# Performance work log

Hardware: AMD Instinct MI355X
Metric: run time of the kernel (lower is better)

## Reference

```python
import jax, jax.numpy as jnp
import numpy as np

DIM = 1024
DEPTH = 4
HEADS = 16
MLP_DIM = 4096
EPS = 1e-5


def layer_norm(x, g, b):
    mu = jnp.mean(x, axis=-1, keepdims=True)
    var = jnp.mean(jnp.square(x - mu), axis=-1, keepdims=True)
    return (x - mu) * jax.lax.rsqrt(var + EPS) * g + b


def setup_inputs() -> dict:
    key = jax.random.key(0)
    ks = jax.random.split(key, 8)
    s = DIM ** -0.5
    return {
        "x": jax.random.normal(ks[0], (2, 1024, DIM), dtype=jnp.float32),
        "ln1_g": jnp.ones((DIM,), jnp.float32),
        "ln1_b": jnp.zeros((DIM,), jnp.float32),
        "w_qkv": jax.random.normal(ks[1], (DIM, 3 * DIM), jnp.float32) * s,
        "w_o": jax.random.normal(ks[2], (DIM, DIM), jnp.float32) * s,
        "b_o": jnp.zeros((DIM,), jnp.float32),
        "ln2_g": jnp.ones((DIM,), jnp.float32),
        "ln2_b": jnp.zeros((DIM,), jnp.float32),
        "w1": jax.random.normal(ks[3], (DIM, MLP_DIM), jnp.float32) * s,
        "b1": jnp.zeros((MLP_DIM,), jnp.float32),
        "w2": jax.random.normal(ks[4], (MLP_DIM, DIM), jnp.float32) * (MLP_DIM ** -0.5),
        "b2": jnp.zeros((DIM,), jnp.float32),
    }


def reference(x, ln1_g, ln1_b, w_qkv, w_o, b_o, ln2_g, ln2_b, w1, b1, w2, b2):
    b, n, _ = x.shape
    h, d = HEADS, DIM // HEADS
    scale = DIM ** -0.5  # NB: full dim, as in source
    for _ in range(DEPTH):  # same (shared) weights each layer, per ModuleList([m]*depth)
        # --- attention with pre-norm + residual ---
        xn = layer_norm(x, ln1_g, ln1_b)
        qkv = xn @ w_qkv  # [b, n, 3*dim]
        qkv = qkv.reshape(b, n, 3, h, d)
        q = qkv[:, :, 0].transpose(0, 2, 1, 3)  # [b, h, n, d]
        k = qkv[:, :, 1].transpose(0, 2, 1, 3)
        v = qkv[:, :, 2].transpose(0, 2, 1, 3)
        scores = jnp.einsum('bhid,bhjd->bhij', q, k) * scale
        attn = jax.nn.softmax(scores, axis=-1)
        out = jnp.einsum('bhij,bhjd->bhid', attn, v)
        out = out.transpose(0, 2, 1, 3).reshape(b, n, DIM)
        x = out @ w_o + b_o + x
        # --- MLP with pre-norm + residual ---
        xn = layer_norm(x, ln2_g, ln2_b)
        hdn = jax.nn.gelu(xn @ w1 + b1, approximate=False)
        x = hdn @ w2 + b2 + x
    return x
```

## Files before the change

### kernel.cpp

```cpp
#include <hip/hip_runtime.h>
#include <math.h>

#define NTOK 2048
#define DIM_ 1024
#define NSEQ 1024
#define HEADS_ 16
#define HD 64
#define MLP_ 4096
#define EPS_ 1e-5f

#define FLAG_BIAS  1
#define FLAG_GELU  2
#define FLAG_QKV   8
#define FLAG_PART  16

typedef __attribute__((ext_vector_type(8))) short bf16x8;
typedef __attribute__((ext_vector_type(4))) float f32x4;
typedef __attribute__((ext_vector_type(16))) float f32x16;

__device__ __forceinline__ unsigned short f2bf(float f) {
    unsigned u = __float_as_uint(f);
    u += 0x7fffu + ((u >> 16) & 1u);
    return (unsigned short)(u >> 16);
}
__device__ __forceinline__ float bf2f(unsigned short u) {
    return __uint_as_float(((unsigned)u) << 16);
}
__device__ __forceinline__ void gld16(const unsigned short* g, short* l) {
    __builtin_amdgcn_global_load_lds(
        (const __attribute__((address_space(1))) void*)g,
        (__attribute__((address_space(3))) void*)l, 16, 0, 0);
}
__device__ __forceinline__ float gelu_fast(float v) {
    float u = 1.5957691f * (v + 0.044715f * v * v * v);
    return v / (1.0f + __expf(-u));
}

__global__ __launch_bounds__(256) void wconv_kernel(const float* __restrict__ W,
                                                    unsigned short* __restrict__ Wt,
                                                    int K, int N,
                                                    float qscale, int qcols) {
    __shared__ float s[32][33];
    int n0 = blockIdx.x * 32, k0 = blockIdx.y * 32;
    int tx = threadIdx.x, ty = threadIdx.y;
    #pragma unroll
    for (int r = 0; r < 4; r++) {
        int k = ty + r * 8;
        s[k][tx] = W[(size_t)(k0 + k) * N + n0 + tx];
    }
    __syncthreads();
    #pragma unroll
    for (int r = 0; r < 4; r++) {
        int n = ty + r * 8;
        float v = s[tx][n];
        if (n0 + n < qcols) v *= qscale;
        Wt[(size_t)(n0 + n) * K + k0 + tx] = f2bf(v);
    }
}

__global__ __launch_bounds__(256) void ln_kernel(const float* __restrict__ src,
                                                 unsigned short* __restrict__ dst,
                                                 const float* __restrict__ g,
                                                 const float* __restrict__ b) {
    int row = blockIdx.x;
    int t = threadIdx.x;
    const float4* x4 = (const float4*)(src + (size_t)row * DIM_);
    float4 f = x4[t];
    float s  = f.x + f.y + f.z + f.w;
    float sq = f.x*f.x + f.y*f.y + f.z*f.z + f.w*f.w;
    __shared__ float ssum[256], ssq[256];
    ssum[t] = s; ssq[t] = sq;
    __syncthreads();
    for (int o = 128; o > 0; o >>= 1) {
        if (t < o) { ssum[t] += ssum[t+o]; ssq[t] += ssq[t+o]; }
        __syncthreads();
    }
    float mu  = ssum[0] * (1.0f / DIM_);
    float var = ssq[0] * (1.0f / DIM_) - mu * mu;
    float r = rsqrtf(var + EPS_);
    const float4* g4 = (const float4*)g;
    const float4* b4 = (const float4*)b;
    float4 gg = g4[t], bb = b4[t];
    ushort4 o4;
    o4.x = f2bf((f.x - mu) * r * gg.x + bb.x);
    o4.y = f2bf((f.y - mu) * r * gg.y + bb.y);
    o4.z = f2bf((f.z - mu) * r * gg.z + bb.z);
    o4.w = f2bf((f.w - mu) * r * gg.w + bb.w);
    ((ushort4*)(dst + (size_t)row * DIM_))[t] = o4;
}

__global__ __launch_bounds__(256) void gemm128_kernel(const unsigned short* __restrict__ A,
                                                      const unsigned short* __restrict__ Bt,
                                                      unsigned short* __restrict__ Cb,
                                                      unsigned short* __restrict__ Vt,
                                                      unsigned short* __restrict__ Ppart,
                                                      const float* __restrict__ bias,
                                                      int M, int N, int K, int KC,
                                                      int ldcb, int nx, int gz, int flags) {
    __shared__ short As[128 * 64];
    __shared__ short Bs[128 * 64];
    int id = blockIdx.x;
    int xcd = id & 7, s = id >> 3;
    int x = s % nx, pl = s / nx;
    int pair = pl * 8 + xcd;
    int z = pair % gz, y = pair / gz;
    int col0 = x * 128, row0 = y * 128;
    int k_beg = z * KC, k_end = k_beg + KC;

    int t = threadIdx.x;
    int lane = t & 63, w = t >> 6;
    int wm = w & 1, wn = w >> 1;

    f32x16 acc[2][2];
    #pragma unroll
    for (int mi = 0; mi < 2; mi++)
        #pragma unroll
        for (int ni = 0; ni < 2; ni++)
            #pragma unroll
            for (int r = 0; r < 16; r++) acc[mi][ni][r] = 0.f;

    int r0 = t >> 3;
    int lchunk = ((t & 7) ^ (r0 & 7)) * 8;
    const unsigned short* Ag = A  + (size_t)(row0 + r0) * K + lchunk;
    const unsigned short* Bg = Bt + (size_t)(col0 + r0) * K + lchunk;
    short* Al = As + t * 8;
    short* Bl = Bs + t * 8;

    int n_l = lane & 31, hi = lane >> 5;
    int x7 = lane & 7;

    for (int k0 = k_beg; k0 < k_end; k0 += 64) {
        #pragma unroll
        for (int i = 0; i < 4; i++) {
            gld16(Ag + k0 + (size_t)i * 32 * K, Al + i * 2048);
            gld16(Bg + k0 + (size_t)i * 32 * K, Bl + i * 2048);
        }
        __syncthreads();

        #pragma unroll
        for (int ks = 0; ks < 4; ks++) {
            int cb = ((ks * 2 + hi) ^ x7) * 8;
            bf16x8 af[2], bfr[2];
            #pragma unroll
            for (int mi = 0; mi < 2; mi++)
                af[mi]  = *(const bf16x8*)&As[(wm * 64 + mi * 32 + n_l) * 64 + cb];
            #pragma unroll
            for (int ni = 0; ni < 2; ni++)
                bfr[ni] = *(const bf16x8*)&Bs[(wn * 64 + ni * 32 + n_l) * 64 + cb];
            #pragma unroll
            for (int mi = 0; mi < 2; mi++)
                #pragma unroll
                for (int ni = 0; ni < 2; ni++)
                    acc[mi][ni] = __builtin_amdgcn_mfma_f32_32x32x16_bf16(af[mi], bfr[ni],
                                                                          acc[mi][ni], 0, 0, 0);
        }
        __syncthreads();
    }

    if (flags & FLAG_PART) {
        unsigned short* P = Ppart + (size_t)z * M * N;
        #pragma unroll
        for (int mi = 0; mi < 2; mi++)
            #pragma unroll
            for (int ni = 0; ni < 2; ni++) {
                int col = col0 + wn * 64 + ni * 32 + n_l;
                #pragma unroll
                for (int reg = 0; reg < 16; reg++) {
                    int row = row0 + wm * 64 + mi * 32 + (reg & 3) + 8 * (reg >> 2) + 4 * hi;
                    P[(size_t)row * N + col] = f2bf(acc[mi][ni][reg]);
                }
            }
        return;
    }

    int colw = col0 + wn * 64;
    if ((flags & FLAG_QKV) && colw >= 2048) {
        int h = (colw - 2048) >> 6;
        #pragma unroll
        for (int mi = 0; mi < 2; mi++)
            #pragma unroll
            for (int g = 0; g < 4; g++) {
                int tok0 = row0 + wm * 64 + mi * 32 + g * 8 + 4 * hi;
                int bb = tok0 >> 10, nn = tok0 & 1023;
                #pragma unroll
                for (int ni = 0; ni < 2; ni++) {
                    int d = ni * 32 + n_l;
                    ushort4 o4;
                    o4.x = f2bf(acc[mi][ni][g * 4 + 0]);
                    o4.y = f2bf(acc[mi][ni][g * 4 + 1]);
                    o4.z = f2bf(acc[mi][ni][g * 4 + 2]);
                    o4.w = f2bf(acc[mi][ni][g * 4 + 3]);
                    *(ushort4*)(Vt + ((size_t)(bb * 16 + h) * 64 + d) * 1024 + nn) = o4;
                }
            }
        return;
    }

    #pragma unroll
    for (int mi = 0; mi < 2; mi++)
        #pragma unroll
        for (int ni = 0; ni < 2; ni++) {
            int col = colw + ni * 32 + n_l;
            float bv = (flags & FLAG_BIAS) ? bias[col] : 0.0f;
            #pragma unroll
            for (int reg = 0; reg < 16; reg++) {
                int row = row0 + wm * 64 + mi * 32 + (reg & 3) + 8 * (reg >> 2) + 4 * hi;
                float v = acc[mi][ni][reg] + bv;
                if (flags & FLAG_GELU) v = gelu_fast(v);
                Cb[(size_t)row * ldcb + col] = f2bf(v);
            }
        }
}

__global__ __launch_bounds__(256) void reduce_ln_kernel(const unsigned short* __restrict__ P,
                                                        int nsplit,
                                                        const float* __restrict__ bias,
                                                        const float* __restrict__ resid,
                                                        float* __restrict__ xc_out,
                                                        unsigned short* __restrict__ xn_out,
                                                        const float* __restrict__ g,
                                                        const float* __restrict__ b) {
    const int MN = NTOK * DIM_;
    int row = blockIdx.x;
    int t = threadIdx.x;
    size_t i = (size_t)row * DIM_ + t * 4;
    float4 y  = *(const float4*)(resid + i);
    float4 bi = *(const float4*)(bias + t * 4);
    y.x += bi.x; y.y += bi.y; y.z += bi.z; y.w += bi.w;
    for (int z = 0; z < nsplit; z++) {
        ushort4 p = *(const ushort4*)(P + (size_t)z * MN + i);
        y.x += bf2f(p.x); y.y += bf2f(p.y); y.z += bf2f(p.z); y.w += bf2f(p.w);
    }
    *(float4*)(xc_out + i) = y;
    if (!xn_out) return;

    float s  = y.x + y.y + y.z + y.w;
    float sq = y.x*y.x + y.y*y.y + y.z*y.z + y.w*y.w;
    __shared__ float ssum[256], ssq[256];
    ssum[t] = s; ssq[t] = sq;
    __syncthreads();
    for (int o = 128; o > 0; o >>= 1) {
        if (t < o) { ssum[t] += ssum[t+o]; ssq[t] += ssq[t+o]; }
        __syncthreads();
    }
    float mu  = ssum[0] * (1.0f / DIM_);
    float var = ssq[0] * (1.0f / DIM_) - mu * mu;
    float r = rsqrtf(var + EPS_);
    float4 gg = *(const float4*)(g + t * 4);
    float4 bb = *(const float4*)(b + t * 4);
    ushort4 o4;
    o4.x = f2bf((y.x - mu) * r * gg.x + bb.x);
    o4.y = f2bf((y.y - mu) * r * gg.y + bb.y);
    o4.z = f2bf((y.z - mu) * r * gg.z + bb.z);
    o4.w = f2bf((y.w - mu) * r * gg.w + bb.w);
    ((ushort4*)(xn_out + (size_t)row * DIM_))[t] = o4;
}

__global__ __launch_bounds__(512) void fattn_kernel(const unsigned short* __restrict__ qk,
                                                    const unsigned short* __restrict__ VtG,
                                                    unsigned short* __restrict__ out) {
    int idx = blockIdx.x;
    int qt = idx >> 5;
    int h  = idx & 15;
    int b  = (idx >> 4) & 1;
    int t  = threadIdx.x;
    int lane = t & 63, w = t >> 6;
    int m = lane & 15, quad = lane >> 4;

    __shared__ unsigned short Ks[2][64 * 64];
    __shared__ unsigned short Vs[2][64 * 64];
    __shared__ unsigned short Ps[8][16 * 72];

    const size_t base = (size_t)b * NSEQ * 2048;
    const int i0 = qt * 128 + w * 16;

    bf16x8 aq0, aq1;
    {
        const unsigned short* qrow = qk + base + (size_t)(i0 + m) * 2048 + h * HD;
        aq0 = *(const bf16x8*)(qrow + quad * 8);
        aq1 = *(const bf16x8*)(qrow + 32 + quad * 8);
    }

    f32x4 Oacc[4];
    #pragma unroll
    for (int dt = 0; dt < 4; dt++) Oacc[dt] = (f32x4){0.f, 0.f, 0.f, 0.f};
    float lsum[4] = {0.f, 0.f, 0.f, 0.f};

    int srow = t >> 3;
    int schunk = t & 7;
    int swc = schunk ^ (srow & 7);
    const unsigned short* Kg = qk + base + 1024 + h * HD + (size_t)srow * 2048 + schunk * 8;
    const unsigned short* Vg = VtG + ((size_t)(b * 16 + h) * 64 + srow) * 1024 + schunk * 8;
    const int sloff = srow * 64 + swc * 8;

    bf16x8 kreg = *(const bf16x8*)(Kg);
    bf16x8 vreg = *(const bf16x8*)(Vg);

    for (int jt = 0; jt < NSEQ / 64; jt++) {
        int cur = jt & 1;
        *(bf16x8*)&Ks[cur][sloff] = kreg;
        *(bf16x8*)&Vs[cur][sloff] = vreg;
        __syncthreads();
        if (jt + 1 < NSEQ / 64) {
            kreg = *(const bf16x8*)(Kg + (size_t)(jt + 1) * 64 * 2048);
            vreg = *(const bf16x8*)(Vg + (jt + 1) * 64);
        }

        f32x4 s[4];
        #pragma unroll
        for (int nt = 0; nt < 4; nt++) {
            int jr = nt * 16 + m;
            const unsigned short* kr = &Ks[cur][jr * 64];
            int x7 = jr & 7;
            bf16x8 b0 = *(const bf16x8*)(kr + (quad ^ x7) * 8);
            bf16x8 b1 = *(const bf16x8*)(kr + ((quad + 4) ^ x7) * 8);
            f32x4 a = (f32x4){0.f, 0.f, 0.f, 0.f};
            a = __builtin_amdgcn_mfma_f32_16x16x32_bf16(aq0, b0, a, 0, 0, 0);
            a = __builtin_amdgcn_mfma_f32_16x16x32_bf16(aq1, b1, a, 0, 0, 0);
            s[nt] = a;
        }

        #pragma unroll
        for (int r = 0; r < 4; r++) {
            float p0 = __expf(s[0][r]);
            float p1 = __expf(s[1][r]);
            float p2 = __expf(s[2][r]);
            float p3 = __expf(s[3][r]);
            lsum[r] += p0 + p1 + p2 + p3;
            unsigned short* pr = &Ps[w][(quad * 4 + r) * 72 + m];
            pr[0]  = f2bf(p0);
            pr[16] = f2bf(p1);
            pr[32] = f2bf(p2);
            pr[48] = f2bf(p3);
        }

        const unsigned short* pa = &Ps[w][m * 72 + quad * 8];
        bf16x8 ap0 = *(const bf16x8*)pa;
        bf16x8 ap1 = *(const bf16x8*)(pa + 32);
        #pragma unroll
        for (int dt = 0; dt < 4; dt++) {
            int dr = dt * 16 + m;
            const unsigned short* vr = &Vs[cur][dr * 64];
            int x7 = dr & 7;
            bf16x8 b0 = *(const bf16x8*)(vr + (quad ^ x7) * 8);
            bf16x8 b1 = *(const bf16x8*)(vr + ((quad + 4) ^ x7) * 8);
            Oacc[dt] = __builtin_amdgcn_mfma_f32_16x16x32_bf16(ap0, b0, Oacc[dt], 0, 0, 0);
            Oacc[dt] = __builtin_amdgcn_mfma_f32_16x16x32_bf16(ap1, b1, Oacc[dt], 0, 0, 0);
        }
    }

    #pragma unroll
    for (int r = 0; r < 4; r++) {
        float rs = lsum[r];
        rs += __shfl_xor(rs, 1);
        rs += __shfl_xor(rs, 2);
        rs += __shfl_xor(rs, 4);
        rs += __shfl_xor(rs, 8);
        lsum[r] = rs;
    }

    #pragma unroll
    for (int r = 0; r < 4; r++) {
        float inv = 1.0f / lsum[r];
        int row = i0 + quad * 4 + r;
        unsigned short* orow = out + ((size_t)(b * NSEQ + row)) * DIM_ + h * HD + m;
        orow[0]  = f2bf(Oacc[0][r] * inv);
        orow[16] = f2bf(Oacc[1][r] * inv);
        orow[32] = f2bf(Oacc[2][r] * inv);
        orow[48] = f2bf(Oacc[3][r] * inv);
    }
}

extern "C" void kernel_launch(void* const* d_in, const int* in_sizes, int n_in,
                              void* d_out, int out_size, void* d_ws, size_t ws_size,
                              hipStream_t stream) {
    const float* x    = (const float*)d_in[0];
    const float* ln1g = (const float*)d_in[1];
    const float* ln1b = (const float*)d_in[2];
    const float* wqkv = (const float*)d_in[3];
    const float* wo   = (const float*)d_in[4];
    const float* bo   = (const float*)d_in[5];
    const float* ln2g = (const float*)d_in[6];
    const float* ln2b = (const float*)d_in[7];
    const float* w1   = (const float*)d_in[8];
    const float* b1   = (const float*)d_in[9];
    const float* w2   = (const float*)d_in[10];
    const float* b2   = (const float*)d_in[11];
    float* out = (float*)d_out;

    char* ws = (char*)d_ws;
    float*          xcur = (float*)(ws);
    unsigned short* aout = (unsigned short*)(ws + (8u<<20));
    unsigned short* xn   = (unsigned short*)(ws + (12u<<20));
    unsigned short* qk   = (unsigned short*)(ws + (16u<<20));
    unsigned short* VtG  = (unsigned short*)(ws + (24u<<20));
    unsigned short* hdn  = (unsigned short*)(ws + (28u<<20));
    unsigned short* wtqkv= (unsigned short*)(ws + (44u<<20));
    unsigned short* wto  = (unsigned short*)(ws + (50u<<20));
    unsigned short* wt1  = (unsigned short*)(ws + (52u<<20));
    unsigned short* wt2  = (unsigned short*)(ws + (60u<<20));
    unsigned short* opart  = (unsigned short*)(ws + (12u<<20));
    unsigned short* m2part = (unsigned short*)(ws + (8u<<20));

    wconv_kernel<<<dim3(3*DIM_/32, DIM_/32), dim3(32,8), 0, stream>>>(wqkv, wtqkv, DIM_, 3*DIM_,
                                                                      0.03125f, DIM_);
    wconv_kernel<<<dim3(DIM_/32,   DIM_/32), dim3(32,8), 0, stream>>>(wo,   wto, DIM_, DIM_, 1.f, 0);
    wconv_kernel<<<dim3(MLP_/32,   DIM_/32), dim3(32,8), 0, stream>>>(w1,   wt1, DIM_, MLP_, 1.f, 0);
    wconv_kernel<<<dim3(DIM_/32,   MLP_/32), dim3(32,8), 0, stream>>>(w2,   wt2, MLP_, DIM_, 1.f, 0);

    for (int layer = 0; layer < 4; layer++) {
        if (layer == 0)
            ln_kernel<<<NTOK, 256, 0, stream>>>(x, xn, ln1g, ln1b);
        gemm128_kernel<<<384, 256, 0, stream>>>(
            xn, wtqkv, qk, VtG, nullptr, nullptr,
            NTOK, 3*DIM_, DIM_, DIM_, 2048, 24, 1, FLAG_QKV);
        fattn_kernel<<<256, 512, 0, stream>>>(qk, VtG, aout);
        gemm128_kernel<<<512, 256, 0, stream>>>(
            aout, wto, nullptr, nullptr, opart, nullptr,
            NTOK, DIM_, DIM_, DIM_/4, 0, 8, 4, FLAG_PART);
        reduce_ln_kernel<<<NTOK, 256, 0, stream>>>(
            opart, 4, bo, (layer == 0 ? x : xcur), xcur, xn, ln2g, ln2b);
        gemm128_kernel<<<512, 256, 0, stream>>>(
            xn, wt1, hdn, nullptr, nullptr, b1,
            NTOK, MLP_, DIM_, DIM_, MLP_, 32, 1, FLAG_BIAS | FLAG_GELU);
        gemm128_kernel<<<512, 256, 0, stream>>>(
            hdn, wt2, nullptr, nullptr, m2part, nullptr,
            NTOK, DIM_, MLP_, MLP_/4, 0, 8, 4, FLAG_PART);
        if (layer < 3)
            reduce_ln_kernel<<<NTOK, 256, 0, stream>>>(
                m2part, 4, b2, xcur, xcur, xn, ln1g, ln1b);
        else
            reduce_ln_kernel<<<NTOK, 256, 0, stream>>>(
                m2part, 4, b2, xcur, out, nullptr, nullptr, nullptr);
    }
}
```

Baseline: 613.0 us.

## Double-buffer GEMM LDS tiles and use two waves with 64x128 warp tiles

Rewrites the 128x128 bf16 MFMA GEMM to run 2 waves per block instead of 4. Each wave now computes a 64x128 tile with 8 accumulators, and the A/B tiles are double-buffered in LDS. The global-to-LDS load of the tile two steps ahead is issued while the current one is consumed, guarded by explicit vmcnt waits and barriers. This aims to hide global load latency and to reuse B fragments across more MFMAs. The cost is doubled LDS (64KB per block), higher register pressure, and fewer waves per CU, which may limit occupancy.

```diff
diff --git a/kernel.cpp b/kernel.cpp
--- a/kernel.cpp
+++ b/kernel.cpp
@@ -89,72 +89,88 @@
     ((ushort4*)(dst + (size_t)row * DIM_))[t] = o4;
 }
 
-__global__ __launch_bounds__(256) void gemm128_kernel(const unsigned short* __restrict__ A,
-                                                      const unsigned short* __restrict__ Bt,
-                                                      unsigned short* __restrict__ Cb,
-                                                      unsigned short* __restrict__ Vt,
-                                                      unsigned short* __restrict__ Ppart,
-                                                      const float* __restrict__ bias,
-                                                      int M, int N, int K, int KC,
-                                                      int ldcb, int nx, int gz, int flags) {
-    __shared__ short As[128 * 64];
-    __shared__ short Bs[128 * 64];
+__global__ __launch_bounds__(128, 2) void gemm128_kernel(const unsigned short* __restrict__ A,
+                                                         const unsigned short* __restrict__ Bt,
+                                                         unsigned short* __restrict__ Cb,
+                                                         unsigned short* __restrict__ Vt,
+                                                         unsigned short* __restrict__ Ppart,
+                                                         const float* __restrict__ bias,
+                                                         int M, int N, int K, int KC,
+                                                         int ldcb, int nx, int gz, int flags) {
+    __shared__ short As[2][128 * 64];
+    __shared__ short Bs[2][128 * 64];
+    const int BUFS = 128 * 64;
+
     int id = blockIdx.x;
     int xcd = id & 7, s = id >> 3;
     int x = s % nx, pl = s / nx;
     int pair = pl * 8 + xcd;
     int z = pair % gz, y = pair / gz;
     int col0 = x * 128, row0 = y * 128;
-    int k_beg = z * KC, k_end = k_beg + KC;
+    int k_beg = z * KC;
+    int nt = KC >> 6;
 
     int t = threadIdx.x;
     int lane = t & 63, w = t >> 6;
-    int wm = w & 1, wn = w >> 1;
-
-    f32x16 acc[2][2];
+    int n_l = lane & 31, hi = lane >> 5;
+    int x7 = lane & 7;
+
+    f32x16 acc[2][4];
     #pragma unroll
     for (int mi = 0; mi < 2; mi++)
         #pragma unroll
-        for (int ni = 0; ni < 2; ni++)
+        for (int ni = 0; ni < 4; ni++)
             #pragma unroll
             for (int r = 0; r < 16; r++) acc[mi][ni][r] = 0.f;
 
     int r0 = t >> 3;
     int lchunk = ((t & 7) ^ (r0 & 7)) * 8;
-    const unsigned short* Ag = A  + (size_t)(row0 + r0) * K + lchunk;
-    const unsigned short* Bg = Bt + (size_t)(col0 + r0) * K + lchunk;
-    short* Al = As + t * 8;
-    short* Bl = Bs + t * 8;
-
-    int n_l = lane & 31, hi = lane >> 5;
-    int x7 = lane & 7;
-
-    for (int k0 = k_beg; k0 < k_end; k0 += 64) {
-        #pragma unroll
-        for (int i = 0; i < 4; i++) {
-            gld16(Ag + k0 + (size_t)i * 32 * K, Al + i * 2048);
-            gld16(Bg + k0 + (size_t)i * 32 * K, Bl + i * 2048);
-        }
-        __syncthreads();
-
+    const unsigned short* Ag = A  + (size_t)(row0 + r0) * K + k_beg + lchunk;
+    const unsigned short* Bg = Bt + (size_t)(col0 + r0) * K + k_beg + lchunk;
+    short* Al = &As[0][t * 8];
+    short* Bl = &Bs[0][t * 8];
+
+    auto stage = [&](int buf_, int tt_) {
+        #pragma unroll
+        for (int i = 0; i < 8; i++) {
+            gld16(Ag + tt_ * 64 + (size_t)i * 16 * K, Al + buf_ * BUFS + i * 1024);
+            gld16(Bg + tt_ * 64 + (size_t)i * 16 * K, Bl + buf_ * BUFS + i * 1024);
+        }
+    };
+    stage(0, 0);
+    if (nt > 1) stage(1, 1);
+
+    for (int tt = 0; tt < nt; tt++) {
+        int cur = tt & 1;
+        if (tt + 1 < nt) asm volatile("s_waitcnt vmcnt(16)" ::: "memory");
+        else             asm volatile("s_waitcnt vmcnt(0)" ::: "memory");
+        __builtin_amdgcn_s_barrier();
+        asm volatile("" ::: "memory");
+
+        const short* Ab = &As[cur][0];
+        const short* Bb = &Bs[cur][0];
         #pragma unroll
         for (int ks = 0; ks < 4; ks++) {
             int cb = ((ks * 2 + hi) ^ x7) * 8;
-            bf16x8 af[2], bfr[2];
+            bf16x8 af[2], bfr[4];
             #pragma unroll
             for (int mi = 0; mi < 2; mi++)
-                af[mi]  = *(const bf16x8*)&As[(wm * 64 + mi * 32 + n_l) * 64 + cb];
-            #pragma unroll
-            for (int ni = 0; ni < 2; ni++)
-                bfr[ni] = *(const bf16x8*)&Bs[(wn * 64 + ni * 32 + n_l) * 64 + cb];
+                af[mi]  = *(const bf16x8*)&Ab[(w * 64 + mi * 32 + n_l) * 64 + cb];
+            #pragma unroll
+            for (int ni = 0; ni < 4; ni++)
+                bfr[ni] = *(const bf16x8*)&Bb[(ni * 32 + n_l) * 64 + cb];
             #pragma unroll
             for (int mi = 0; mi < 2; mi++)
                 #pragma unroll
-                for (int ni = 0; ni < 2; ni++)
+                for (int ni = 0; ni < 4; ni++)
                     acc[mi][ni] = __builtin_amdgcn_mfma_f32_32x32x16_bf16(af[mi], bfr[ni],
                                                                           acc[mi][ni], 0, 0, 0);
         }
-        __syncthreads();
+
+        asm volatile("" ::: "memory");
+        __builtin_amdgcn_s_barrier();
+        asm volatile("" ::: "memory");
+        if (tt + 2 < nt) stage(cur, tt + 2);
     }
 
     if (flags & FLAG_PART) {
@@ -162,29 +178,28 @@
         #pragma unroll
         for (int mi = 0; mi < 2; mi++)
             #pragma unroll
-            for (int ni = 0; ni < 2; ni++) {
-                int col = col0 + wn * 64 + ni * 32 + n_l;
+            for (int ni = 0; ni < 4; ni++) {
+                int col = col0 + ni * 32 + n_l;
                 #pragma unroll
                 for (int reg = 0; reg < 16; reg++) {
-                    int row = row0 + wm * 64 + mi * 32 + (reg & 3) + 8 * (reg >> 2) + 4 * hi;
+                    int row = row0 + w * 64 + mi * 32 + (reg & 3) + 8 * (reg >> 2) + 4 * hi;
                     P[(size_t)row * N + col] = f2bf(acc[mi][ni][reg]);
                 }
             }
         return;
     }
 
-    int colw = col0 + wn * 64;
-    if ((flags & FLAG_QKV) && colw >= 2048) {
-        int h = (colw - 2048) >> 6;
+    if ((flags & FLAG_QKV) && col0 >= 2048) {
         #pragma unroll
         for (int mi = 0; mi < 2; mi++)
             #pragma unroll
             for (int g = 0; g < 4; g++) {
-                int tok0 = row0 + wm * 64 + mi * 32 + g * 8 + 4 * hi;
+                int tok0 = row0 + w * 64 + mi * 32 + g * 8 + 4 * hi;
                 int bb = tok0 >> 10, nn = tok0 & 1023;
                 #pragma unroll
-                for (int ni = 0; ni < 2; ni++) {
-                    int d = ni * 32 + n_l;
+                for (int ni = 0; ni < 4; ni++) {
+                    int cg = col0 - 2048 + ni * 32 + n_l;
+                    int h = cg >> 6, d = cg & 63;
                     ushort4 o4;
                     o4.x = f2bf(acc[mi][ni][g * 4 + 0]);
                     o4.y = f2bf(acc[mi][ni][g * 4 + 1]);
@@ -199,12 +214,12 @@
     #pragma unroll
     for (int mi = 0; mi < 2; mi++)
         #pragma unroll
-        for (int ni = 0; ni < 2; ni++) {
-            int col = colw + ni * 32 + n_l;
+        for (int ni = 0; ni < 4; ni++) {
+            int col = col0 + ni * 32 + n_l;
             float bv = (flags & FLAG_BIAS) ? bias[col] : 0.0f;
             #pragma unroll
             for (int reg = 0; reg < 16; reg++) {
-                int row = row0 + wm * 64 + mi * 32 + (reg & 3) + 8 * (reg >> 2) + 4 * hi;
+                int row = row0 + w * 64 + mi * 32 + (reg & 3) + 8 * (reg >> 2) + 4 * hi;
                 float v = acc[mi][ni][reg] + bv;
                 if (flags & FLAG_GELU) v = gelu_fast(v);
                 Cb[(size_t)row * ldcb + col] = f2bf(v);
@@ -411,19 +426,19 @@
     for (int layer = 0; layer < 4; layer++) {
         if (layer == 0)
             ln_kernel<<<NTOK, 256, 0, stream>>>(x, xn, ln1g, ln1b);
-        gemm128_kernel<<<384, 256, 0, stream>>>(
+        gemm128_kernel<<<384, 128, 0, stream>>>(
             xn, wtqkv, qk, VtG, nullptr, nullptr,
             NTOK, 3*DIM_, DIM_, DIM_, 2048, 24, 1, FLAG_QKV);
         fattn_kernel<<<256, 512, 0, stream>>>(qk, VtG, aout);
-        gemm128_kernel<<<512, 256, 0, stream>>>(
+        gemm128_kernel<<<512, 128, 0, stream>>>(
             aout, wto, nullptr, nullptr, opart, nullptr,
             NTOK, DIM_, DIM_, DIM_/4, 0, 8, 4, FLAG_PART);
         reduce_ln_kernel<<<NTOK, 256, 0, stream>>>(
             opart, 4, bo, (layer == 0 ? x : xcur), xcur, xn, ln2g, ln2b);
-        gemm128_kernel<<<512, 256, 0, stream>>>(
+        gemm128_kernel<<<512, 128, 0, stream>>>(
             xn, wt1, hdn, nullptr, nullptr, b1,
             NTOK, MLP_, DIM_, DIM_, MLP_, 32, 1, FLAG_BIAS | FLAG_GELU);
-        gemm128_kernel<<<512, 256, 0, stream>>>(
+        gemm128_kernel<<<512, 128, 0, stream>>>(
             hdn, wt2, nullptr, nullptr, m2part, nullptr,
             NTOK, DIM_, MLP_, MLP_/4, 0, 8, 4, FLAG_PART);
         if (layer < 3)
```

Measured after the change: 666.8 us. 1.09x slower.
